# Performance work log

Measured on AMD Instinct MI355X. Metric: run time of the kernel, lower is better.

Reference implementation:

```python
import jax, jax.numpy as jnp
import numpy as np

B, N, P, Q, E = 8, 5000, 256, 256, 160000


def _linear_params(k, out_d, in_d):
    # matches nn.init.normal_(std=0.1) weights, zero bias
    return 0.1 * jax.random.normal(k, (out_d, in_d), jnp.float32), jnp.zeros((out_d,), jnp.float32)


def setup_inputs() -> dict:
    key = jax.random.key(0)
    ks = jax.random.split(key, 8)
    u = jax.random.normal(ks[0], (B, N, P + Q), jnp.float32)
    src = jax.random.randint(ks[1], (E,), 0, N, dtype=jnp.int32)
    dst = jax.random.randint(ks[2], (E,), 0, N, dtype=jnp.int32)
    t = jnp.zeros((1,), jnp.float32)
    W_Fc, b_Fc = _linear_params(ks[3], P, P + Q)
    W_Fh, b_Fh = _linear_params(ks[4], Q, P + Q)
    W_Gc, b_Gc = _linear_params(ks[5], P, P + Q)
    W_Z, b_Z = _linear_params(ks[6], P, P + Q)
    W_A, b_A = _linear_params(ks[7], Q, 2 * Q)
    return dict(u=u, src=src, dst=dst, t=t,
                W_Fc=W_Fc, b_Fc=b_Fc, W_Fh=W_Fh, b_Fh=b_Fh,
                W_Gc=W_Gc, b_Gc=b_Gc, W_Z=W_Z, b_Z=b_Z,
                W_A=W_A, b_A=b_A)


def _neighbor_mean(h, src, dst):
    # h: [B, N, Q] -> mean over in-neighbors per node (zeros if no neighbors)
    hT = jnp.transpose(h, (1, 0, 2))            # [N, B, Q]
    msgs = hT[src]                              # [E, B, Q] gather
    summed = jax.ops.segment_sum(msgs, dst, num_segments=N)          # [N, B, Q]
    deg = jax.ops.segment_sum(jnp.ones((E,), h.dtype), dst, num_segments=N)  # [N]
    mean = summed / jnp.maximum(deg, 1.0)[:, None, None]
    return jnp.transpose(mean, (1, 0, 2))       # [B, N, Q]


def reference(u, src, dst, t, W_Fc, b_Fc, W_Fh, b_Fh, W_Gc, b_Gc, W_Z, b_Z, W_A, b_A):
    sp = jax.nn.softplus
    lin = lambda x, W, b: jnp.einsum('bnd,od->bno', x, W) + b
    c = u[:, :, :P]
    h = u[:, :, P:]
    agg = _neighbor_mean(h, src, dst)                           # [B, N, Q]
    h_ = sp(lin(jnp.concatenate([h, agg], axis=2), W_A, b_A))   # [B, N, Q]
    u_ = jnp.concatenate([c, h_], axis=2)                       # [B, N, P+Q]
    Fc = sp(lin(u_, W_Fc, b_Fc))
    Gc = sp(lin(u_, W_Gc, b_Gc))
    Zt = jnp.tanh(lin(u_, W_Z, b_Z))
    Fh = sp(lin(u_, W_Fh, b_Fh))
    dc = -Fc * c + Gc * Zt
    dh = -Fh * h
    # tangent projection: remove component of dc along c
    proj = jnp.sum(dc * c, axis=2, keepdims=True) / jnp.sum(c * c, axis=2, keepdims=True)
    dc = dc - proj * c
    return jnp.concatenate([dc, dh], axis=2)
```

## Files before the change

kernel.cpp:

```cpp
#include <hip/hip_runtime.h>
#include <math.h>

#define B_ 8
#define N_ 5000
#define E_ 160000
#define M_ 40000
#define K_ 512
#define XT_ 313
#define CAP_ 128

typedef __bf16 v8bf __attribute__((ext_vector_type(8)));
typedef float  v4f  __attribute__((ext_vector_type(4)));
typedef unsigned short u16x4v __attribute__((ext_vector_type(4)));
typedef unsigned short u16x8v __attribute__((ext_vector_type(8)));

__device__ __forceinline__ unsigned short f2b(float f){
  unsigned int u = __builtin_bit_cast(unsigned int, f);
  u += 0x7FFFu + ((u >> 16) & 1u);
  return (unsigned short)(u >> 16);
}
__device__ __forceinline__ float b2f(unsigned short s){
  return __builtin_bit_cast(float, ((unsigned int)s) << 16);
}
__device__ __forceinline__ float softplus_(float x){
  return (x > 15.0f) ? x : __logf(1.0f + __expf(x));
}
__device__ __forceinline__ float tanh_(float x){
  float e = __expf(2.0f*x);
  return 1.0f - 2.0f/(e + 1.0f);
}

__global__ __launch_bounds__(256) void prep_kernel(
    const float* __restrict__ u,
    const float* __restrict__ wA, const float* __restrict__ wFc,
    const float* __restrict__ wGc, const float* __restrict__ wZ,
    const float* __restrict__ wFh,
    const float* __restrict__ bFc, const float* __restrict__ bGc,
    const float* __restrict__ bZ,  const float* __restrict__ bFh,
    unsigned short* __restrict__ cB, unsigned short* __restrict__ hT,
    unsigned short* __restrict__ WA, unsigned short* __restrict__ Wall,
    float* __restrict__ biasP, int* __restrict__ cursor)
{
  const int bid = blockIdx.x;
  if (bid < 10000){
    int r = bid*4 + (threadIdx.x >> 6);
    int l = threadIdx.x & 63;
    int n = r >> 3, b = r & 7;
    const float* up = u + (size_t)(b*N_ + n)*512 + l*4;
    float4 cf = *(const float4*)up;
    float4 hf = *(const float4*)(up + 256);
    u16x4v c4, h4;
    c4.x = f2b(cf.x); c4.y = f2b(cf.y); c4.z = f2b(cf.z); c4.w = f2b(cf.w);
    h4.x = f2b(hf.x); h4.y = f2b(hf.y); h4.z = f2b(hf.z); h4.w = f2b(hf.w);
    *(u16x4v*)(cB + (size_t)r*256 + l*4) = c4;
    *(u16x4v*)(hT + (size_t)r*256 + l*4) = h4;
    return;
  }
  if (bid < 12564){
    int idx = (bid - 10000)*256 + threadIdx.x;
    if (idx >= 655360){
      int j = idx - 655360;
      int mat = j >> 8, jj = j & 255;
      const float* bp = (mat == 0) ? bFc : (mat == 1) ? bGc : (mat == 2) ? bZ : bFh;
      biasP[j] = bp[jj];
      return;
    }
    int m = idx >> 17;
    int i = idx & 131071;
    float v;
    if      (m == 0) v = wA[i];
    else if (m == 1) v = wFc[i];
    else if (m == 2) v = wGc[i];
    else if (m == 3) v = wZ[i];
    else             v = wFh[i];
    unsigned short o = f2b(v);
    int n   = (m == 0) ? (i >> 9) : ((m - 1)*256 + (i >> 9));
    int col = i & 511;
    int y  = n >> 7, nn = n & 127;
    int cb = nn >> 4, lr = nn & 15;
    int kb = col >> 6, c6 = col & 63;
    int ch = c6 >> 3, e = c6 & 7;
    int ks = ch >> 2, lq = ch & 3;
    int lane = lq*16 + lr;
    size_t pidx = ((((size_t)(y*8 + kb)*2 + ks)*8 + cb)*64 + lane)*8 + e;
    if (m == 0) WA[pidx] = o;
    else        Wall[pidx] = o;
    return;
  }
  int i = (bid - 12564)*256 + threadIdx.x;
  if (i < N_) cursor[i] = 0;
}

__global__ __launch_bounds__(256) void fill_direct(
    const int* __restrict__ src, const int* __restrict__ dst,
    int* __restrict__ cursor, int* __restrict__ csr)
{
  int e = blockIdx.x*256 + threadIdx.x;
  int d = dst[e];
  int p = atomicAdd(&cursor[d], 1);
  if (p < CAP_) csr[d*CAP_ + p] = src[e];
}

__global__ __launch_bounds__(256) void gather_bn_kernel(
    const unsigned short* __restrict__ hT, const int* __restrict__ csr,
    const int* __restrict__ cursor, unsigned short* __restrict__ aggT)
{
  const int id = blockIdx.x;
  const int bb = id & 7;
  const int g  = id >> 3;
  const int tid = threadIdx.x;
  const int n = g*4 + (tid >> 6);
  const int l = tid & 63;
  const int half = l >> 5, li = l & 31;
  const size_t coff = (size_t)bb*256 + li*8;
  const int cnt = min(cursor[n], CAP_);
  const int base = n*CAP_;

  float acc[8] = {};
  int e = 0;
  for (; e + 3 < cnt; e += 4){
    const int s0 = csr[base + e + half];
    const int s1 = csr[base + e + 2 + half];
    u16x8v v0 = *(const u16x8v*)(hT + (size_t)s0*2048 + coff);
    u16x8v v1 = *(const u16x8v*)(hT + (size_t)s1*2048 + coff);
#pragma unroll
    for (int i = 0; i < 8; ++i) acc[i] += b2f(v0[i]) + b2f(v1[i]);
  }
  for (; e < cnt; e += 2){
    const int idx = e + half;
    u16x8v v = {};
    if (idx < cnt){
      const int s = csr[base + idx];
      v = *(const u16x8v*)(hT + (size_t)s*2048 + coff);
    }
#pragma unroll
    for (int i = 0; i < 8; ++i) acc[i] += b2f(v[i]);
  }
#pragma unroll
  for (int i = 0; i < 8; ++i) acc[i] += __shfl_xor(acc[i], 32, 64);

  if (half == 0){
    const float inv = 1.0f / (float)((cnt > 1) ? cnt : 1);
    u16x8v o;
#pragma unroll
    for (int i = 0; i < 8; ++i) o[i] = f2b(acc[i]*inv);
    *(u16x8v*)(aggT + (size_t)n*2048 + coff) = o;
  }
}


__device__ __forceinline__ void stage_a(
    const unsigned short* __restrict__ As, int m0, int ak,
    int srow, int schunk, int w, unsigned short* lbuf)
{
#pragma unroll
  for (int i = 0; i < 4; ++i){
    const unsigned short* gp = As + (size_t)(m0 + i*32 + srow)*256 + ak + schunk*8;
    unsigned short* lp = lbuf + (i*32 + w*8)*64;
    __builtin_amdgcn_global_load_lds((const __attribute__((address_space(1))) void*)gp,
                                     (__attribute__((address_space(3))) void*)lp, 16, 0, 0);
  }
}

__device__ __forceinline__ void load_b(
    const unsigned short* __restrict__ Bp, int y, int kb, int wc, int l, v8bf (&b)[8])
{
#pragma unroll
  for (int ks = 0; ks < 2; ++ks)
#pragma unroll
    for (int ct = 0; ct < 4; ++ct)
      b[ks*4+ct] = *(const v8bf*)(Bp +
          ((((size_t)(y*8 + kb)*2 + ks)*8 + wc*4 + ct)*64 + l)*8);
}

__device__ __forceinline__ void compute_tile(
    const unsigned short* lA, int wr, int lq, int lr,
    const v8bf (&bb)[8], v4f (&acc)[4][4])
{
#pragma unroll
  for (int ks = 0; ks < 2; ++ks){
    v8bf a[4];
#pragma unroll
    for (int rt = 0; rt < 4; ++rt){
      const int ar = wr*64 + rt*16 + lr;
      a[rt] = *(const v8bf*)(lA + ar*64 + (((ks*4 + lq) ^ (ar & 7)))*8);
    }
#pragma unroll
    for (int rt = 0; rt < 4; ++rt)
#pragma unroll
      for (int ct = 0; ct < 4; ++ct)
        acc[rt][ct] = __builtin_amdgcn_mfma_f32_16x16x32_bf16(a[rt], bb[ks*4+ct], acc[rt][ct], 0, 0, 0);
  }
}

template<int MODE>
__global__ __launch_bounds__(256, 3) void gemm_tiled(
    const unsigned short* __restrict__ A0, const unsigned short* __restrict__ A1,
    const unsigned short* __restrict__ Bp, const float* __restrict__ bias,
    unsigned short* dstp)
{
  const int id = blockIdx.x;
  int x, y;
  if (MODE == 1){
    const int u6 = id & 63;
    y = u6 >> 3;
    x = (id >> 6)*8 + (u6 & 7);
  } else {
    const int u4 = id & 15;
    y = u4 >> 3;
    x = (id >> 4)*8 + (u4 & 7);
  }
  if (x >= XT_) return;

  __shared__ unsigned short lds[24576];

  const int tid = threadIdx.x;
  const int w  = tid >> 6, l = tid & 63;
  const int wr = w >> 1,  wc = w & 1;
  const int lq = l >> 4,  lr = l & 15;
  const int m0 = x * 128;
  const int n0 = y * 128;

  const int srow   = tid >> 3;
  const int schunk = (tid & 7) ^ (srow & 7);

  v4f acc[4][4] = {};
  v8bf b0[8], b1[8];

  stage_a(A0, m0, 0,  srow, schunk, w, lds);
  asm volatile("" ::: "memory");
  load_b(Bp, y, 0, wc, l, b0);
  asm volatile("" ::: "memory");
  stage_a(A0, m0, 64, srow, schunk, w, lds + 8192);
  asm volatile("s_waitcnt vmcnt(12)" ::: "memory");
  __builtin_amdgcn_s_barrier();
  __builtin_amdgcn_sched_barrier(0);

#pragma unroll
  for (int kb = 0; kb < 7; ++kb){
    const int kp = kb + 2;
    if (kp < 8)
      stage_a((kp < 4) ? A0 : A1, m0, (kp & 3)*64, srow, schunk, w,
              lds + (kp % 3)*8192);
    asm volatile("" ::: "memory");
    if ((kb + 1) & 1) load_b(Bp, y, kb + 1, wc, l, b1);
    else              load_b(Bp, y, kb + 1, wc, l, b0);
    if (kb & 1) compute_tile(lds + (kb % 3)*8192, wr, lq, lr, b1, acc);
    else        compute_tile(lds + (kb % 3)*8192, wr, lq, lr, b0, acc);
    asm volatile("s_waitcnt vmcnt(12)" ::: "memory");
    __builtin_amdgcn_s_barrier();
    __builtin_amdgcn_sched_barrier(0);
  }
  compute_tile(lds + 8192, wr, lq, lr, b1, acc);

  float bv[4];
#pragma unroll
  for (int ct = 0; ct < 4; ++ct) bv[ct] = bias[n0 + wc*64 + ct*16 + lr];

  __syncthreads();
#pragma unroll
  for (int rt = 0; rt < 4; ++rt){
#pragma unroll
    for (int ct = 0; ct < 4; ++ct){
      const int col = wc*64 + ct*16 + lr;
#pragma unroll
      for (int reg = 0; reg < 4; ++reg){
        const int row = wr*64 + rt*16 + lq*4 + reg;
        const float xv = acc[rt][ct][reg] + bv[ct];
        const float v = (MODE == 0) ? softplus_(xv) : xv;
        lds[row*136 + col] = f2b(v);
      }
    }
  }
  __syncthreads();

#pragma unroll
  for (int i = 0; i < 8; ++i){
    const int row = i*16 + (tid >> 4);
    const int r = m0 + row;
    if (r < M_){
      const uint4 v = *(const uint4*)(lds + row*136 + (tid & 15)*8);
      if (MODE == 0){
        *(uint4*)(dstp + (size_t)r*256 + n0 + (tid & 15)*8) = v;
      } else {
        const int n = r >> 3, b = r & 7;
        *(uint4*)(dstp + ((size_t)b*N_ + n)*1024 + n0 + (tid & 15)*8) = v;
      }
    }
  }
}


__global__ __launch_bounds__(256) void epilogue_kernel(
    const unsigned short* act, const float* __restrict__ u, float* out)
{
  int r = blockIdx.x*4 + (threadIdx.x >> 6);
  int l = threadIdx.x & 63;
  int n = r >> 3, b = r & 7;
  const size_t rr = (size_t)(b*N_ + n);
  const unsigned short* arow = act + rr*1024;
  const float* urow = u + rr*512;
  float* orow = out + rr*512;

  u16x4v fc4 = *(const u16x4v*)(arow +        l*4);
  u16x4v gc4 = *(const u16x4v*)(arow + 256 +  l*4);
  u16x4v z4  = *(const u16x4v*)(arow + 512 +  l*4);
  u16x4v fh4 = *(const u16x4v*)(arow + 768 +  l*4);
  float4 c4f = *(const float4*)(urow + l*4);
  float4 h4f = *(const float4*)(urow + 256 + l*4);

  float c[4] = {c4f.x, c4f.y, c4f.z, c4f.w};
  float h[4] = {h4f.x, h4f.y, h4f.z, h4f.w};
  float dc[4], fh[4];
  float num = 0.f, den = 0.f;
#pragma unroll
  for (int i = 0; i < 4; ++i){
    float fc = softplus_(b2f(fc4[i]));
    float gc = softplus_(b2f(gc4[i]));
    float z  = tanh_(b2f(z4[i]));
    fh[i] = softplus_(b2f(fh4[i]));
    dc[i] = -fc*c[i] + gc*z;
    num += dc[i]*c[i];
    den += c[i]*c[i];
  }
#pragma unroll
  for (int s = 1; s < 64; s <<= 1){
    num += __shfl_xor(num, s, 64);
    den += __shfl_xor(den, s, 64);
  }
  const float proj = num / den;

  float4 o, oh;
  o.x = dc[0] - proj*c[0]; o.y = dc[1] - proj*c[1];
  o.z = dc[2] - proj*c[2]; o.w = dc[3] - proj*c[3];
  oh.x = -fh[0]*h[0]; oh.y = -fh[1]*h[1];
  oh.z = -fh[2]*h[2]; oh.w = -fh[3]*h[3];
  *(float4*)(orow + l*4) = o;
  *(float4*)(orow + 256 + l*4) = oh;
}


extern "C" void kernel_launch(void* const* d_in, const int* in_sizes, int n_in,
                              void* d_out, int out_size, void* d_ws, size_t ws_size,
                              hipStream_t stream) {
  const float* u    = (const float*)d_in[0];
  const int*   src  = (const int*)d_in[1];
  const int*   dst  = (const int*)d_in[2];
  const float* wFc  = (const float*)d_in[4];
  const float* bFc  = (const float*)d_in[5];
  const float* wFh  = (const float*)d_in[6];
  const float* bFh  = (const float*)d_in[7];
  const float* wGc  = (const float*)d_in[8];
  const float* bGc  = (const float*)d_in[9];
  const float* wZ   = (const float*)d_in[10];
  const float* bZ   = (const float*)d_in[11];
  const float* wA   = (const float*)d_in[12];
  const float* bA   = (const float*)d_in[13];
  float* out = (float*)d_out;
  unsigned short* act = (unsigned short*)d_out;

  char* W = (char*)d_ws;
  unsigned short* hT   = (unsigned short*)(W + 0);
  unsigned short* cB   = (unsigned short*)(W + 20480000);
  unsigned short* aggT = (unsigned short*)(W + 40960000);
  unsigned short* hB   = (unsigned short*)(W + 61440000);
  int* csr             = (int*)(W + 61440000);
  unsigned short* WA   = (unsigned short*)(W + 81920000);
  unsigned short* Wall = (unsigned short*)(W + 82182144);
  float* biasP   = (float*)(W + 83230720);
  int* cursor    = (int*)(W + 83234816);

  prep_kernel<<<12584, 256, 0, stream>>>(u, wA, wFc, wGc, wZ, wFh,
                                         bFc, bGc, bZ, bFh,
                                         cB, hT, WA, Wall, biasP, cursor);
  fill_direct<<<E_/256, 256, 0, stream>>>(src, dst, cursor, csr);
  gather_bn_kernel<<<8*1250, 256, 0, stream>>>(hT, csr, cursor, aggT);

  gemm_tiled<0><<<40*16, 256, 0, stream>>>(hT, aggT, WA, bA, hB);
  gemm_tiled<1><<<40*64, 256, 0, stream>>>(cB, hB, Wall, biasP, act);

  epilogue_kernel<<<M_/4, 256, 0, stream>>>(act, u, out);
}
```

Baseline: 316.9 us.

## Widen prep/epilogue vector accesses and split second GEMM into two launches

New measurement: 319.8 us. Within noise of the previous version (+0.9%).

```diff
diff --git a/kernel.cpp b/kernel.cpp
--- a/kernel.cpp
+++ b/kernel.cpp
@@ -43,17 +43,18 @@
 {
   const int bid = blockIdx.x;
   if (bid < 10000){
-    int r = bid*4 + (threadIdx.x >> 6);
-    int l = threadIdx.x & 63;
-    int n = r >> 3, b = r & 7;
-    const float* up = u + (size_t)(b*N_ + n)*512 + l*4;
-    float4 cf = *(const float4*)up;
-    float4 hf = *(const float4*)(up + 256);
-    u16x4v c4, h4;
-    c4.x = f2b(cf.x); c4.y = f2b(cf.y); c4.z = f2b(cf.z); c4.w = f2b(cf.w);
-    h4.x = f2b(hf.x); h4.y = f2b(hf.y); h4.z = f2b(hf.z); h4.w = f2b(hf.w);
-    *(u16x4v*)(cB + (size_t)r*256 + l*4) = c4;
-    *(u16x4v*)(hT + (size_t)r*256 + l*4) = h4;
+    const int r = bid*4 + (threadIdx.x >> 6);
+    const int l = threadIdx.x & 63;
+    const int half = l >> 5, li = l & 31;
+    const int n = r >> 3, b = r & 7;
+    const float* up = u + (size_t)(b*N_ + n)*512 + half*256 + li*8;
+    float4 f0 = *(const float4*)up;
+    float4 f1 = *(const float4*)(up + 4);
+    u16x8v o;
+    o[0] = f2b(f0.x); o[1] = f2b(f0.y); o[2] = f2b(f0.z); o[3] = f2b(f0.w);
+    o[4] = f2b(f1.x); o[5] = f2b(f1.y); o[6] = f2b(f1.z); o[7] = f2b(f1.w);
+    unsigned short* dstp = half ? hT : cB;
+    *(u16x8v*)(dstp + (size_t)r*256 + li*8) = o;
     return;
   }
   if (bid < 12564){
@@ -197,14 +198,14 @@
 __global__ __launch_bounds__(256, 3) void gemm_tiled(
     const unsigned short* __restrict__ A0, const unsigned short* __restrict__ A1,
     const unsigned short* __restrict__ Bp, const float* __restrict__ bias,
-    unsigned short* dstp)
+    unsigned short* dstp, int y0)
 {
   const int id = blockIdx.x;
   int x, y;
   if (MODE == 1){
-    const int u6 = id & 63;
-    y = u6 >> 3;
-    x = (id >> 6)*8 + (u6 & 7);
+    const int u5 = id & 31;
+    y = y0 + (u5 >> 3);
+    x = (id >> 5)*8 + (id & 7);
   } else {
     const int u4 = id & 15;
     y = u4 >> 3;
@@ -290,53 +291,59 @@
   }
 }
 
-
 __global__ __launch_bounds__(256) void epilogue_kernel(
     const unsigned short* act, const float* __restrict__ u, float* out)
 {
-  int r = blockIdx.x*4 + (threadIdx.x >> 6);
-  int l = threadIdx.x & 63;
-  int n = r >> 3, b = r & 7;
+  const int tid = threadIdx.x;
+  const int w = tid >> 6, l = tid & 63;
+  const int half = l >> 5, li = l & 31;
+  const int r = blockIdx.x*8 + w*2 + half;
+  const int n = r >> 3, b = r & 7;
   const size_t rr = (size_t)(b*N_ + n);
   const unsigned short* arow = act + rr*1024;
   const float* urow = u + rr*512;
   float* orow = out + rr*512;
-
-  u16x4v fc4 = *(const u16x4v*)(arow +        l*4);
-  u16x4v gc4 = *(const u16x4v*)(arow + 256 +  l*4);
-  u16x4v z4  = *(const u16x4v*)(arow + 512 +  l*4);
-  u16x4v fh4 = *(const u16x4v*)(arow + 768 +  l*4);
-  float4 c4f = *(const float4*)(urow + l*4);
-  float4 h4f = *(const float4*)(urow + 256 + l*4);
-
-  float c[4] = {c4f.x, c4f.y, c4f.z, c4f.w};
-  float h[4] = {h4f.x, h4f.y, h4f.z, h4f.w};
-  float dc[4], fh[4];
+  const int q0 = li*8;
+
+  u16x8v fc8 = *(const u16x8v*)(arow +        q0);
+  u16x8v gc8 = *(const u16x8v*)(arow + 256 +  q0);
+  u16x8v z8  = *(const u16x8v*)(arow + 512 +  q0);
+  u16x8v fh8 = *(const u16x8v*)(arow + 768 +  q0);
+  float4 c4a = *(const float4*)(urow + q0);
+  float4 c4b = *(const float4*)(urow + q0 + 4);
+  float4 h4a = *(const float4*)(urow + 256 + q0);
+  float4 h4b = *(const float4*)(urow + 256 + q0 + 4);
+
+  float c[8] = {c4a.x,c4a.y,c4a.z,c4a.w,c4b.x,c4b.y,c4b.z,c4b.w};
+  float h[8] = {h4a.x,h4a.y,h4a.z,h4a.w,h4b.x,h4b.y,h4b.z,h4b.w};
+  float dc[8], fh[8];
   float num = 0.f, den = 0.f;
 #pragma unroll
-  for (int i = 0; i < 4; ++i){
-    float fc = softplus_(b2f(fc4[i]));
-    float gc = softplus_(b2f(gc4[i]));
-    float z  = tanh_(b2f(z4[i]));
-    fh[i] = softplus_(b2f(fh4[i]));
+  for (int i = 0; i < 8; ++i){
+    float fc = softplus_(b2f(fc8[i]));
+    float gc = softplus_(b2f(gc8[i]));
+    float z  = tanh_(b2f(z8[i]));
+    fh[i] = softplus_(b2f(fh8[i]));
     dc[i] = -fc*c[i] + gc*z;
     num += dc[i]*c[i];
     den += c[i]*c[i];
   }
 #pragma unroll
-  for (int s = 1; s < 64; s <<= 1){
+  for (int s = 1; s < 32; s <<= 1){
     num += __shfl_xor(num, s, 64);
     den += __shfl_xor(den, s, 64);
   }
   const float proj = num / den;
 
-  float4 o, oh;
-  o.x = dc[0] - proj*c[0]; o.y = dc[1] - proj*c[1];
-  o.z = dc[2] - proj*c[2]; o.w = dc[3] - proj*c[3];
-  oh.x = -fh[0]*h[0]; oh.y = -fh[1]*h[1];
-  oh.z = -fh[2]*h[2]; oh.w = -fh[3]*h[3];
-  *(float4*)(orow + l*4) = o;
-  *(float4*)(orow + 256 + l*4) = oh;
+  float4 oa, ob, ha, hb;
+  oa.x = dc[0]-proj*c[0]; oa.y = dc[1]-proj*c[1]; oa.z = dc[2]-proj*c[2]; oa.w = dc[3]-proj*c[3];
+  ob.x = dc[4]-proj*c[4]; ob.y = dc[5]-proj*c[5]; ob.z = dc[6]-proj*c[6]; ob.w = dc[7]-proj*c[7];
+  ha.x = -fh[0]*h[0]; ha.y = -fh[1]*h[1]; ha.z = -fh[2]*h[2]; ha.w = -fh[3]*h[3];
+  hb.x = -fh[4]*h[4]; hb.y = -fh[5]*h[5]; hb.z = -fh[6]*h[6]; hb.w = -fh[7]*h[7];
+  *(float4*)(orow + q0)       = oa;
+  *(float4*)(orow + q0 + 4)   = ob;
+  *(float4*)(orow + 256 + q0)     = ha;
+  *(float4*)(orow + 256 + q0 + 4) = hb;
 }
 
 
@@ -376,8 +383,9 @@
   fill_direct<<<E_/256, 256, 0, stream>>>(src, dst, cursor, csr);
   gather_bn_kernel<<<8*1250, 256, 0, stream>>>(hT, csr, cursor, aggT);
 
-  gemm_tiled<0><<<40*16, 256, 0, stream>>>(hT, aggT, WA, bA, hB);
-  gemm_tiled<1><<<40*64, 256, 0, stream>>>(cB, hB, Wall, biasP, act);
-
-  epilogue_kernel<<<M_/4, 256, 0, stream>>>(act, u, out);
-}
+  gemm_tiled<0><<<40*16, 256, 0, stream>>>(hT, aggT, WA, bA, hB, 0);
+  gemm_tiled<1><<<40*32, 256, 0, stream>>>(cB, hB, Wall, biasP, act, 0);
+  gemm_tiled<1><<<40*32, 256, 0, stream>>>(cB, hB, Wall, biasP, act, 4);
+
+  epilogue_kernel<<<M_/8, 256, 0, stream>>>(act, u, out);
+}
```
